# Kernel optimization log

Hardware: AMD Instinct MI355X
Metric: run time of the kernel (lower is better)

Reference implementation:

```python
import jax, jax.numpy as jnp
import numpy as np

THRESH = 0.5
MARGIN = 0.1
SCALE_POS = 2.0
SCALE_NEG = 40.0
SCALE_POS_W = 1.0
SCALE_NEG_W = 1.0

B, D = 4096, 256
N_CLASSES = 64


def setup_inputs() -> dict:
    key = jax.random.key(0)
    k1, k2, k3 = jax.random.split(key, 3)
    feats = jax.random.normal(k1, (B, D), dtype=jnp.float32)
    sim_weight = jax.random.uniform(k2, (B, B), dtype=jnp.float32)
    labels = jax.random.randint(k3, (B,), 0, N_CLASSES, dtype=jnp.int64)
    return {"feats": feats, "sim_weight": sim_weight, "labels": labels}


def reference(feats, sim_weight, labels):
    # L2-normalize rows, cosine-similarity matrix [B, B]
    feats_norm = feats / jnp.linalg.norm(feats, axis=1, keepdims=True)
    sim = feats_norm @ feats_norm.T

    # pos mask includes the diagonal (labels[i] == labels[i]), matching torch code
    pos_mask = labels[:, None] == labels[None, :]
    neg_mask = ~pos_mask

    # per-row min positive similarity (pos set is never empty due to diagonal)
    min_pos = jnp.min(jnp.where(pos_mask, sim, jnp.inf), axis=1, keepdims=True)
    # per-row max negative similarity; only valid when row has a negative
    has_neg = jnp.any(neg_mask, axis=1, keepdims=True)
    max_neg = jnp.max(jnp.where(neg_mask, sim, -jnp.inf), axis=1, keepdims=True)

    # hard mining: keep negs harder than the easiest pos, pos harder than hardest neg
    neg_keep = neg_mask & (sim + MARGIN > min_pos)
    pos_keep = pos_mask & jnp.where(has_neg, sim - MARGIN < max_neg, True)

    # masked log-sum-exp style reductions (non-vanila path uses sim_weight)
    pos_exp = jnp.exp(-SCALE_POS * (sim - THRESH) + SCALE_POS_W * sim_weight)
    neg_exp = jnp.exp(SCALE_NEG * (sim - THRESH) - SCALE_NEG_W * sim_weight)
    pos_sum = jnp.sum(jnp.where(pos_keep, pos_exp, 0.0), axis=1)
    neg_sum = jnp.sum(jnp.where(neg_keep, neg_exp, 0.0), axis=1)

    pos_loss = jnp.log1p(pos_sum) / SCALE_POS
    neg_loss = jnp.log1p(neg_sum) / SCALE_NEG
    # rows with both sets empty contribute log1p(0)=0, matching the `continue`
    return jnp.sum(pos_loss + neg_loss) / feats.shape[0]
```

## Files before the change

### kernel.cpp

```cpp
#include <hip/hip_runtime.h>
#include <hip/hip_bf16.h>
#include <math.h>

#define B_SZ 4096
#define D_SZ 256
#define MARGIN   0.1f

typedef __attribute__((ext_vector_type(8))) __bf16 bf16x8;
typedef __attribute__((ext_vector_type(4))) float f32x4;
typedef __attribute__((ext_vector_type(8))) unsigned short u16x8;

__device__ __forceinline__ unsigned fmap(float f) {
    unsigned u = __float_as_uint(f);
    return (u & 0x80000000u) ? ~u : (u | 0x80000000u);
}
__device__ __forceinline__ float funmap(unsigned u) {
    return (u & 0x80000000u) ? __uint_as_float(u ^ 0x80000000u)
                             : __uint_as_float(~u);
}
#define MINPOS_INIT 0xFF800000u
#define MAXNEG_INIT 0x007FFFFFu

__device__ __forceinline__ unsigned short f2bf(float f) {
    unsigned u = __float_as_uint(f);
    unsigned r = (u + 0x7FFFu + ((u >> 16) & 1u)) >> 16;
    return (unsigned short)r;
}

__device__ __forceinline__ void gload_lds16(const void* g, void* lds) {
    __builtin_amdgcn_global_load_lds(
        (const __attribute__((address_space(1))) void*)g,
        (__attribute__((address_space(3))) void*)lds, 16, 0, 0);
}

__global__ void norm_init_kernel(const float* __restrict__ feats,
                                 unsigned short* __restrict__ fb,
                                 unsigned* __restrict__ minpos,
                                 unsigned* __restrict__ maxneg,
                                 float* __restrict__ possum,
                                 float* __restrict__ negsum) {
    int row = blockIdx.x;
    int lane = threadIdx.x;
    const float4 v = *(const float4*)(feats + (size_t)row * D_SZ + lane * 4);
    float s = v.x * v.x + v.y * v.y + v.z * v.z + v.w * v.w;
#pragma unroll
    for (int m = 32; m; m >>= 1) s += __shfl_xor(s, m);
    float rinv = 1.0f / sqrtf(s);
    short4 st;
    st.x = (short)f2bf(v.x * rinv);
    st.y = (short)f2bf(v.y * rinv);
    st.z = (short)f2bf(v.z * rinv);
    st.w = (short)f2bf(v.w * rinv);
    *(short4*)(fb + (size_t)row * D_SZ + lane * 4) = st;
    if (lane == 0) {
        minpos[row] = MINPOS_INIT;
        maxneg[row] = MAXNEG_INIT;
        possum[row] = 0.f;
        negsum[row] = 0.f;
    }
}

__device__ __forceinline__ void gemm_tile(const unsigned short* __restrict__ fb,
                                          unsigned short* lA0, unsigned short* lB0,
                                          int i0, int j0, int t, f32x4 acc[4][4]) {
    const int lane = t & 63, w = t >> 6;
    const int wr = w >> 1, wc = w & 1;
    const int fr = lane & 15, kg = lane >> 4;
    const int srow = lane >> 2, schunk = lane & 3;

#pragma unroll
    for (int m = 0; m < 4; ++m)
#pragma unroll
        for (int n = 0; n < 4; ++n) acc[m][n] = (f32x4){0.f, 0.f, 0.f, 0.f};

    auto stage = [&](int buf, int kc) {
#pragma unroll
        for (int half = 0; half < 2; ++half) {
            const int R0 = w * 32 + half * 16;
            const int row = R0 + srow;
            const int off = ((schunk ^ ((row >> 1) & 3)) << 3);
            gload_lds16(fb + (size_t)(i0 + row) * D_SZ + kc + off,
                        lA0 + buf * (128 * 32) + R0 * 32);
            gload_lds16(fb + (size_t)(j0 + row) * D_SZ + kc + off,
                        lB0 + buf * (128 * 32) + R0 * 32);
        }
    };

    stage(0, 0);
    asm volatile("s_waitcnt vmcnt(0)" ::: "memory");
    __syncthreads();

#pragma unroll
    for (int s = 0; s < 8; ++s) {
        const int cur = s & 1;
        if (s < 7) stage(cur ^ 1, (s + 1) * 32);
        const unsigned short* A  = lA0 + cur * (128 * 32);
        const unsigned short* Bp = lB0 + cur * (128 * 32);
        bf16x8 a[4], b[4];
#pragma unroll
        for (int m = 0; m < 4; ++m) {
            const int row = wr * 64 + m * 16 + fr;
            a[m] = *(const bf16x8*)(A + row * 32 + ((kg ^ ((row >> 1) & 3)) << 3));
        }
#pragma unroll
        for (int n = 0; n < 4; ++n) {
            const int row = wc * 64 + n * 16 + fr;
            b[n] = *(const bf16x8*)(Bp + row * 32 + ((kg ^ ((row >> 1) & 3)) << 3));
        }
#pragma unroll
        for (int m = 0; m < 4; ++m)
#pragma unroll
            for (int n = 0; n < 4; ++n)
                acc[m][n] = __builtin_amdgcn_mfma_f32_16x16x32_bf16(a[m], b[n], acc[m][n], 0, 0, 0);
        if (s < 7) {
            asm volatile("s_waitcnt vmcnt(0)" ::: "memory");
            __syncthreads();
        }
    }
}

__global__ __launch_bounds__(256, 4) void gemm_store(const unsigned short* __restrict__ fb,
                                                     unsigned short* __restrict__ simb) {
    __shared__ unsigned short lA[2 * 128 * 32];
    __shared__ unsigned short lB[2 * 128 * 32];
    const int t = threadIdx.x;
    const int i0 = blockIdx.y * 128, j0 = blockIdx.x * 128;
    f32x4 acc[4][4];
    gemm_tile(fb, lA, lB, i0, j0, t, acc);
    const int lane = t & 63, w = t >> 6;
    const int wr = w >> 1, wc = w & 1, fr = lane & 15, kg = lane >> 4;
#pragma unroll
    for (int m = 0; m < 4; ++m)
#pragma unroll
        for (int r = 0; r < 4; ++r) {
            const size_t row = i0 + wr * 64 + m * 16 + kg * 4 + r;
#pragma unroll
            for (int n = 0; n < 4; ++n)
                simb[row * B_SZ + j0 + wc * 64 + n * 16 + fr] = f2bf(acc[m][n][r]);
        }
}

__global__ __launch_bounds__(256) void row_pass(const unsigned short* __restrict__ simb,
                                                const float* __restrict__ simw,
                                                const int* __restrict__ labels,
                                                float* __restrict__ rowloss) {
    const int i = blockIdx.x, t = threadIdx.x;
    const int lane = t & 63, w = t >> 6;
    const int il = labels[i];
    float sv[16], wv[16];
    int lj[16];
    {
        const u16x8* sp = (const u16x8*)(simb + (size_t)i * B_SZ + t * 16);
        u16x8 s0 = sp[0], s1 = sp[1];
#pragma unroll
        for (int e = 0; e < 8; ++e) {
            sv[e]     = __uint_as_float((unsigned)s0[e] << 16);
            sv[8 + e] = __uint_as_float((unsigned)s1[e] << 16);
        }
        const float4* wp = (const float4*)(simw + (size_t)i * B_SZ + t * 16);
#pragma unroll
        for (int q = 0; q < 4; ++q) {
            float4 wq = wp[q];
            wv[q * 4 + 0] = wq.x; wv[q * 4 + 1] = wq.y;
            wv[q * 4 + 2] = wq.z; wv[q * 4 + 3] = wq.w;
        }
        const int4* lp = (const int4*)(labels + t * 16);
#pragma unroll
        for (int q = 0; q < 4; ++q) {
            int4 lq = lp[q];
            lj[q * 4 + 0] = lq.x; lj[q * 4 + 1] = lq.y;
            lj[q * 4 + 2] = lq.z; lj[q * 4 + 3] = lq.w;
        }
    }
    float mn = INFINITY, mx = -INFINITY;
#pragma unroll
    for (int e = 0; e < 16; ++e) {
        if (lj[e] == il) mn = fminf(mn, sv[e]);
        else             mx = fmaxf(mx, sv[e]);
    }
#pragma unroll
    for (int msk = 1; msk < 64; msk <<= 1) {
        mn = fminf(mn, __shfl_xor(mn, msk));
        mx = fmaxf(mx, __shfl_xor(mx, msk));
    }
    __shared__ float smn[4], smx[4], sps[4], sns[4];
    if (lane == 0) { smn[w] = mn; smx[w] = mx; }
    __syncthreads();
    mn = fminf(fminf(smn[0], smn[1]), fminf(smn[2], smn[3]));
    mx = fmaxf(fmaxf(smx[0], smx[1]), fmaxf(smx[2], smx[3]));
    const bool hasneg = (mx != -INFINITY);
    float ps = 0.f, ns = 0.f;
#pragma unroll
    for (int e = 0; e < 16; ++e) {
        const float s = sv[e];
        if (lj[e] == il) {
            if (!hasneg || (s - MARGIN < mx))
                ps += __expf(fmaf(-2.f, s, 1.f) + wv[e]);
        } else {
            if (s + MARGIN > mn)
                ns += __expf(fmaf(40.f, s, -20.f) - wv[e]);
        }
    }
#pragma unroll
    for (int msk = 1; msk < 64; msk <<= 1) {
        ps += __shfl_xor(ps, msk);
        ns += __shfl_xor(ns, msk);
    }
    if (lane == 0) { sps[w] = ps; sns[w] = ns; }
    __syncthreads();
    if (t == 0) {
        ps = sps[0] + sps[1] + sps[2] + sps[3];
        ns = sns[0] + sns[1] + sns[2] + sns[3];
        rowloss[i] = log1pf(ps) * 0.5f + log1pf(ns) * 0.025f;
    }
}

__global__ void final_big(const float* __restrict__ rowloss, float* __restrict__ out) {
    __shared__ float red[256];
    int t = threadIdx.x;
    float acc = 0.f;
    for (int i = t; i < B_SZ; i += 256) acc += rowloss[i];
    red[t] = acc;
    __syncthreads();
    for (int s = 128; s > 0; s >>= 1) {
        if (t < s) red[t] += red[t + s];
        __syncthreads();
    }
    if (t == 0) out[0] = red[0] / (float)B_SZ;
}

template <int PHASE>
__global__ __launch_bounds__(256) void sim_pass(
    const unsigned short* __restrict__ fb,
    const int* __restrict__ labels,
    const float* __restrict__ simw,
    unsigned* __restrict__ minpos, unsigned* __restrict__ maxneg,
    float* __restrict__ possum, float* __restrict__ negsum) {
    __shared__ unsigned short lA[128 * 64];
    __shared__ unsigned short lB[128 * 64];
    const int t = threadIdx.x;
    const int lane = t & 63, w = t >> 6;
    const int wr = w >> 1, wc = w & 1;
    const int i0 = blockIdx.y * 128, j0 = blockIdx.x * 128;
    const int fr = lane & 15, kg = lane >> 4;
    const int srow = lane >> 3;
    const int scol = ((lane & 7) ^ srow) * 8;

    f32x4 acc[4][4];
#pragma unroll
    for (int m = 0; m < 4; ++m)
#pragma unroll
        for (int n = 0; n < 4; ++n)
            acc[m][n] = (f32x4){0.f, 0.f, 0.f, 0.f};

    const char* pA = (const char*)lA + (wr * 64 + fr) * 128;
    const char* pB = (const char*)lB + (wc * 64 + fr) * 128;
    const int q = (kg * 16) ^ ((fr & 7) << 4);

    for (int kc = 0; kc < D_SZ; kc += 64) {
        __syncthreads();
#pragma unroll
        for (int inst = 0; inst < 4; ++inst) {
            const int r8 = w * 32 + inst * 8;
            gload_lds16(fb + (size_t)(i0 + r8 + srow) * D_SZ + kc + scol, lA + r8 * 64);
            gload_lds16(fb + (size_t)(j0 + r8 + srow) * D_SZ + kc + scol, lB + r8 * 64);
        }
        asm volatile("s_waitcnt vmcnt(0)" ::: "memory");
        __syncthreads();
#pragma unroll
        for (int kk = 0; kk < 2; ++kk) {
            const int off = q ^ (kk * 64);
            bf16x8 a[4], b[4];
#pragma unroll
            for (int m = 0; m < 4; ++m)
                a[m] = *(const bf16x8*)(pA + m * 2048 + off);
#pragma unroll
            for (int n = 0; n < 4; ++n)
                b[n] = *(const bf16x8*)(pB + n * 2048 + off);
#pragma unroll
            for (int m = 0; m < 4; ++m)
#pragma unroll
                for (int n = 0; n < 4; ++n)
                    acc[m][n] = __builtin_amdgcn_mfma_f32_16x16x32_bf16(a[m], b[n], acc[m][n], 0, 0, 0);
        }
    }

    const int iBase = i0 + wr * 64, jBase = j0 + wc * 64;
    int jLab[4];
#pragma unroll
    for (int n = 0; n < 4; ++n) jLab[n] = labels[jBase + n * 16 + fr];

#pragma unroll
    for (int m = 0; m < 4; ++m) {
#pragma unroll
        for (int r = 0; r < 4; ++r) {
            const int i = iBase + m * 16 + kg * 4 + r;
            const int il = labels[i];
            if (PHASE == 0) {
                float mn = INFINITY, mx = -INFINITY;
#pragma unroll
                for (int n = 0; n < 4; ++n) {
                    float s = acc[m][n][r];
                    if (il == jLab[n]) mn = fminf(mn, s);
                    else               mx = fmaxf(mx, s);
                }
#pragma unroll
                for (int msk = 1; msk < 16; msk <<= 1) {
                    mn = fminf(mn, __shfl_xor(mn, msk));
                    mx = fmaxf(mx, __shfl_xor(mx, msk));
                }
                if (fr == 0) {
                    if (mn != INFINITY)  atomicMin(&minpos[i], fmap(mn));
                    if (mx != -INFINITY) atomicMax(&maxneg[i], fmap(mx));
                }
            } else {
                const unsigned mnu = maxneg[i];
                const float minp = funmap(minpos[i]);
                const bool hasneg = (mnu != MAXNEG_INIT);
                const float maxn = funmap(mnu);
                const float* wrow = simw + (size_t)i * B_SZ + jBase + fr;
                float ps = 0.f, ns = 0.f;
#pragma unroll
                for (int n = 0; n < 4; ++n) {
                    float s = acc[m][n][r];
                    float wv = wrow[n * 16];
                    if (il == jLab[n]) {
                        if (!hasneg || (s - MARGIN < maxn))
                            ps += __expf(fmaf(-2.f, s, 1.f) + wv);
                    } else {
                        if (s + MARGIN > minp)
                            ns += __expf(fmaf(40.f, s, -20.f) - wv);
                    }
                }
#pragma unroll
                for (int msk = 1; msk < 16; msk <<= 1) {
                    ps += __shfl_xor(ps, msk);
                    ns += __shfl_xor(ns, msk);
                }
                if (fr == 0) {
                    if (ps != 0.f) atomicAdd(&possum[i], ps);
                    if (ns != 0.f) atomicAdd(&negsum[i], ns);
                }
            }
        }
    }
}

__global__ void final_fb(const float* __restrict__ possum,
                         const float* __restrict__ negsum,
                         float* __restrict__ out) {
    __shared__ float red[256];
    int t = threadIdx.x;
    float acc = 0.f;
    for (int i = t; i < B_SZ; i += 256)
        acc += log1pf(possum[i]) * 0.5f + log1pf(negsum[i]) * 0.025f;
    red[t] = acc;
    __syncthreads();
    for (int s = 128; s > 0; s >>= 1) {
        if (t < s) red[t] += red[t + s];
        __syncthreads();
    }
    if (t == 0) out[0] = red[0] / (float)B_SZ;
}

extern "C" void kernel_launch(void* const* d_in, const int* in_sizes, int n_in,
                              void* d_out, int out_size, void* d_ws, size_t ws_size,
                              hipStream_t stream) {
    const float* feats  = (const float*)d_in[0];
    const float* simw   = (const float*)d_in[1];
    const int*   labels = (const int*)d_in[2];
    float* out = (float*)d_out;

    char* ws = (char*)d_ws;
    unsigned* minpos  = (unsigned*)ws;
    unsigned* maxneg  = (unsigned*)(ws + 1 * B_SZ * 4);
    float*    possum  = (float*)(ws + 2 * B_SZ * 4);
    float*    negsum  = (float*)(ws + 3 * B_SZ * 4);
    float*    rowloss = (float*)(ws + 4 * B_SZ * 4);
    unsigned short* fb   = (unsigned short*)(ws + 5 * B_SZ * 4);
    unsigned short* simb = (unsigned short*)(ws + 5 * B_SZ * 4 + (size_t)B_SZ * D_SZ * 2);

    const size_t NEED_BIG = 5ull * B_SZ * 4 + (size_t)B_SZ * D_SZ * 2
                          + (size_t)B_SZ * B_SZ * 2;

    norm_init_kernel<<<B_SZ, 64, 0, stream>>>(feats, fb, minpos, maxneg, possum, negsum);

    if (ws_size >= NEED_BIG) {
        dim3 grid(B_SZ / 128, B_SZ / 128);
        gemm_store<<<grid, 256, 0, stream>>>(fb, simb);
        row_pass<<<B_SZ, 256, 0, stream>>>(simb, simw, labels, rowloss);
        final_big<<<1, 256, 0, stream>>>(rowloss, out);
    } else {
        dim3 grid(B_SZ / 128, B_SZ / 128);
        sim_pass<0><<<grid, 256, 0, stream>>>(fb, labels, simw, minpos, maxneg, possum, negsum);
        sim_pass<1><<<grid, 256, 0, stream>>>(fb, labels, simw, minpos, maxneg, possum, negsum);
        final_fb<<<1, 256, 0, stream>>>(possum, negsum, out);
    }
}
```

Before: 52.28 us.

## Exploit similarity symmetry: compute upper-triangle tiles and write transposed copies

Replaces the full 32x32 tile GEMM with a triangular launch of 528 blocks that computes only the upper-triangle tiles of the symmetric cosine-similarity matrix. Each off-diagonal block writes its tile directly and also transposes it through swizzled LDS to write the mirrored tile. The intent is to nearly halve the MFMA work and the feature-tile loads. The fallback two-pass atomic path and its workspace init are removed, so the code now assumes the workspace is large enough. It adds a serial loop per block to decode the tile index and an extra LDS round trip plus a second set of stores.

```diff
diff --git a/kernel.cpp b/kernel.cpp
--- a/kernel.cpp
+++ b/kernel.cpp
@@ -9,17 +9,6 @@
 typedef __attribute__((ext_vector_type(8))) __bf16 bf16x8;
 typedef __attribute__((ext_vector_type(4))) float f32x4;
 typedef __attribute__((ext_vector_type(8))) unsigned short u16x8;
-
-__device__ __forceinline__ unsigned fmap(float f) {
-    unsigned u = __float_as_uint(f);
-    return (u & 0x80000000u) ? ~u : (u | 0x80000000u);
-}
-__device__ __forceinline__ float funmap(unsigned u) {
-    return (u & 0x80000000u) ? __uint_as_float(u ^ 0x80000000u)
-                             : __uint_as_float(~u);
-}
-#define MINPOS_INIT 0xFF800000u
-#define MAXNEG_INIT 0x007FFFFFu
 
 __device__ __forceinline__ unsigned short f2bf(float f) {
     unsigned u = __float_as_uint(f);
@@ -34,11 +23,7 @@
 }
 
 __global__ void norm_init_kernel(const float* __restrict__ feats,
-                                 unsigned short* __restrict__ fb,
-                                 unsigned* __restrict__ minpos,
-                                 unsigned* __restrict__ maxneg,
-                                 float* __restrict__ possum,
-                                 float* __restrict__ negsum) {
+                                 unsigned short* __restrict__ fb) {
     int row = blockIdx.x;
     int lane = threadIdx.x;
     const float4 v = *(const float4*)(feats + (size_t)row * D_SZ + lane * 4);
@@ -52,12 +37,6 @@
     st.z = (short)f2bf(v.z * rinv);
     st.w = (short)f2bf(v.w * rinv);
     *(short4*)(fb + (size_t)row * D_SZ + lane * 4) = st;
-    if (lane == 0) {
-        minpos[row] = MINPOS_INIT;
-        maxneg[row] = MAXNEG_INIT;
-        possum[row] = 0.f;
-        negsum[row] = 0.f;
-    }
 }
 
 __device__ __forceinline__ void gemm_tile(const unsigned short* __restrict__ fb,
@@ -119,16 +98,22 @@
     }
 }
 
-__global__ __launch_bounds__(256, 4) void gemm_store(const unsigned short* __restrict__ fb,
-                                                     unsigned short* __restrict__ simb) {
-    __shared__ unsigned short lA[2 * 128 * 32];
-    __shared__ unsigned short lB[2 * 128 * 32];
+__global__ __launch_bounds__(256, 4) void gemm_store_sym(const unsigned short* __restrict__ fb,
+                                                         unsigned short* __restrict__ simb) {
+    __shared__ unsigned short sm[2 * 128 * 32 * 2];
     const int t = threadIdx.x;
-    const int i0 = blockIdx.y * 128, j0 = blockIdx.x * 128;
+
+    int z = blockIdx.x, bi = 0;
+    while (z >= 32 - bi) { z -= 32 - bi; ++bi; }
+    const int bj = bi + z;
+    const int i0 = bi * 128, j0 = bj * 128;
+
     f32x4 acc[4][4];
-    gemm_tile(fb, lA, lB, i0, j0, t, acc);
+    gemm_tile(fb, sm, sm + 128 * 32 * 2, i0, j0, t, acc);
+
     const int lane = t & 63, w = t >> 6;
     const int wr = w >> 1, wc = w & 1, fr = lane & 15, kg = lane >> 4;
+
 #pragma unroll
     for (int m = 0; m < 4; ++m)
 #pragma unroll
@@ -138,6 +123,34 @@
             for (int n = 0; n < 4; ++n)
                 simb[row * B_SZ + j0 + wc * 64 + n * 16 + fr] = f2bf(acc[m][n][r]);
         }
+
+    if (bi == bj) return;
+
+    __syncthreads();
+    unsigned short* T = sm;
+#pragma unroll
+    for (int m = 0; m < 4; ++m) {
+        const int rowbase = wr * 64 + m * 16 + kg * 4;
+#pragma unroll
+        for (int n = 0; n < 4; ++n) {
+            const int col = wc * 64 + n * 16 + fr;
+            short4 h;
+            h.x = (short)f2bf(acc[m][n][0]);
+            h.y = (short)f2bf(acc[m][n][1]);
+            h.z = (short)f2bf(acc[m][n][2]);
+            h.w = (short)f2bf(acc[m][n][3]);
+            *(short4*)(T + col * 128 + (rowbase ^ ((col & 15) << 3))) = h;
+        }
+    }
+    __syncthreads();
+
+    const int r0 = t & 15, cb = t >> 4;
+#pragma unroll
+    for (int p = 0; p < 8; ++p) {
+        const int c = cb + p * 16;
+        u16x8 v = *(const u16x8*)(T + c * 128 + 8 * (r0 ^ (c & 15)));
+        *(u16x8*)(simb + (size_t)(j0 + c) * B_SZ + i0 + r0 * 8) = v;
+    }
 }
 
 __global__ __launch_bounds__(256) void row_pass(const unsigned short* __restrict__ simb,
@@ -229,140 +242,6 @@
     if (t == 0) out[0] = red[0] / (float)B_SZ;
 }
 
-template <int PHASE>
-__global__ __launch_bounds__(256) void sim_pass(
-    const unsigned short* __restrict__ fb,
-    const int* __restrict__ labels,
-    const float* __restrict__ simw,
-    unsigned* __restrict__ minpos, unsigned* __restrict__ maxneg,
-    float* __restrict__ possum, float* __restrict__ negsum) {
-    __shared__ unsigned short lA[128 * 64];
-    __shared__ unsigned short lB[128 * 64];
-    const int t = threadIdx.x;
-    const int lane = t & 63, w = t >> 6;
-    const int wr = w >> 1, wc = w & 1;
-    const int i0 = blockIdx.y * 128, j0 = blockIdx.x * 128;
-    const int fr = lane & 15, kg = lane >> 4;
-    const int srow = lane >> 3;
-    const int scol = ((lane & 7) ^ srow) * 8;
-
-    f32x4 acc[4][4];
-#pragma unroll
-    for (int m = 0; m < 4; ++m)
-#pragma unroll
-        for (int n = 0; n < 4; ++n)
-            acc[m][n] = (f32x4){0.f, 0.f, 0.f, 0.f};
-
-    const char* pA = (const char*)lA + (wr * 64 + fr) * 128;
-    const char* pB = (const char*)lB + (wc * 64 + fr) * 128;
-    const int q = (kg * 16) ^ ((fr & 7) << 4);
-
-    for (int kc = 0; kc < D_SZ; kc += 64) {
-        __syncthreads();
-#pragma unroll
-        for (int inst = 0; inst < 4; ++inst) {
-            const int r8 = w * 32 + inst * 8;
-            gload_lds16(fb + (size_t)(i0 + r8 + srow) * D_SZ + kc + scol, lA + r8 * 64);
-            gload_lds16(fb + (size_t)(j0 + r8 + srow) * D_SZ + kc + scol, lB + r8 * 64);
-        }
-        asm volatile("s_waitcnt vmcnt(0)" ::: "memory");
-        __syncthreads();
-#pragma unroll
-        for (int kk = 0; kk < 2; ++kk) {
-            const int off = q ^ (kk * 64);
-            bf16x8 a[4], b[4];
-#pragma unroll
-            for (int m = 0; m < 4; ++m)
-                a[m] = *(const bf16x8*)(pA + m * 2048 + off);
-#pragma unroll
-            for (int n = 0; n < 4; ++n)
-                b[n] = *(const bf16x8*)(pB + n * 2048 + off);
-#pragma unroll
-            for (int m = 0; m < 4; ++m)
-#pragma unroll
-                for (int n = 0; n < 4; ++n)
-                    acc[m][n] = __builtin_amdgcn_mfma_f32_16x16x32_bf16(a[m], b[n], acc[m][n], 0, 0, 0);
-        }
-    }
-
-    const int iBase = i0 + wr * 64, jBase = j0 + wc * 64;
-    int jLab[4];
-#pragma unroll
-    for (int n = 0; n < 4; ++n) jLab[n] = labels[jBase + n * 16 + fr];
-
-#pragma unroll
-    for (int m = 0; m < 4; ++m) {
-#pragma unroll
-        for (int r = 0; r < 4; ++r) {
-            const int i = iBase + m * 16 + kg * 4 + r;
-            const int il = labels[i];
-            if (PHASE == 0) {
-                float mn = INFINITY, mx = -INFINITY;
-#pragma unroll
-                for (int n = 0; n < 4; ++n) {
-                    float s = acc[m][n][r];
-                    if (il == jLab[n]) mn = fminf(mn, s);
-                    else               mx = fmaxf(mx, s);
-                }
-#pragma unroll
-                for (int msk = 1; msk < 16; msk <<= 1) {
-                    mn = fminf(mn, __shfl_xor(mn, msk));
-                    mx = fmaxf(mx, __shfl_xor(mx, msk));
-                }
-                if (fr == 0) {
-                    if (mn != INFINITY)  atomicMin(&minpos[i], fmap(mn));
-                    if (mx != -INFINITY) atomicMax(&maxneg[i], fmap(mx));
-                }
-            } else {
-                const unsigned mnu = maxneg[i];
-                const float minp = funmap(minpos[i]);
-                const bool hasneg = (mnu != MAXNEG_INIT);
-                const float maxn = funmap(mnu);
-                const float* wrow = simw + (size_t)i * B_SZ + jBase + fr;
-                float ps = 0.f, ns = 0.f;
-#pragma unroll
-                for (int n = 0; n < 4; ++n) {
-                    float s = acc[m][n][r];
-                    float wv = wrow[n * 16];
-                    if (il == jLab[n]) {
-                        if (!hasneg || (s - MARGIN < maxn))
-                            ps += __expf(fmaf(-2.f, s, 1.f) + wv);
-                    } else {
-                        if (s + MARGIN > minp)
-                            ns += __expf(fmaf(40.f, s, -20.f) - wv);
-                    }
-                }
-#pragma unroll
-                for (int msk = 1; msk < 16; msk <<= 1) {
-                    ps += __shfl_xor(ps, msk);
-                    ns += __shfl_xor(ns, msk);
-                }
-                if (fr == 0) {
-                    if (ps != 0.f) atomicAdd(&possum[i], ps);
-                    if (ns != 0.f) atomicAdd(&negsum[i], ns);
-                }
-            }
-        }
-    }
-}
-
-__global__ void final_fb(const float* __restrict__ possum,
-                         const float* __restrict__ negsum,
-                         float* __restrict__ out) {
-    __shared__ float red[256];
-    int t = threadIdx.x;
-    float acc = 0.f;
-    for (int i = t; i < B_SZ; i += 256)
-        acc += log1pf(possum[i]) * 0.5f + log1pf(negsum[i]) * 0.025f;
-    red[t] = acc;
-    __syncthreads();
-    for (int s = 128; s > 0; s >>= 1) {
-        if (t < s) red[t] += red[t + s];
-        __syncthreads();
-    }
-    if (t == 0) out[0] = red[0] / (float)B_SZ;
-}
-
 extern "C" void kernel_launch(void* const* d_in, const int* in_sizes, int n_in,
                               void* d_out, int out_size, void* d_ws, size_t ws_size,
                               hipStream_t stream) {
@@ -372,28 +251,13 @@
     float* out = (float*)d_out;
 
     char* ws = (char*)d_ws;
-    unsigned* minpos  = (unsigned*)ws;
-    unsigned* maxneg  = (unsigned*)(ws + 1 * B_SZ * 4);
-    float*    possum  = (float*)(ws + 2 * B_SZ * 4);
-    float*    negsum  = (float*)(ws + 3 * B_SZ * 4);
-    float*    rowloss = (float*)(ws + 4 * B_SZ * 4);
-    unsigned short* fb   = (unsigned short*)(ws + 5 * B_SZ * 4);
-    unsigned short* simb = (unsigned short*)(ws + 5 * B_SZ * 4 + (size_t)B_SZ * D_SZ * 2);
-
-    const size_t NEED_BIG = 5ull * B_SZ * 4 + (size_t)B_SZ * D_SZ * 2
-                          + (size_t)B_SZ * B_SZ * 2;
-
-    norm_init_kernel<<<B_SZ, 64, 0, stream>>>(feats, fb, minpos, maxneg, possum, negsum);
-
-    if (ws_size >= NEED_BIG) {
-        dim3 grid(B_SZ / 128, B_SZ / 128);
-        gemm_store<<<grid, 256, 0, stream>>>(fb, simb);
-        row_pass<<<B_SZ, 256, 0, stream>>>(simb, simw, labels, rowloss);
-        final_big<<<1, 256, 0, stream>>>(rowloss, out);
-    } else {
-        dim3 grid(B_SZ / 128, B_SZ / 128);
-        sim_pass<0><<<grid, 256, 0, stream>>>(fb, labels, simw, minpos, maxneg, possum, negsum);
-        sim_pass<1><<<grid, 256, 0, stream>>>(fb, labels, simw, minpos, maxneg, possum, negsum);
-        final_fb<<<1, 256, 0, stream>>>(possum, negsum, out);
-    }
-}
+    float*    rowloss = (float*)ws;
+    unsigned short* fb   = (unsigned short*)(ws + B_SZ * 4);
+    unsigned short* simb = (unsigned short*)(ws + B_SZ * 4 + (size_t)B_SZ * D_SZ * 2);
+
+    norm_init_kernel<<<B_SZ, 64, 0, stream>>>(feats, fb);
+
+    gemm_store_sym<<<528, 256, 0, stream>>>(fb, simb);
+    row_pass<<<B_SZ, 256, 0, stream>>>(simb, simw, labels, rowloss);
+    final_big<<<1, 256, 0, stream>>>(rowloss, out);
+}
```

After: 49.88 us. 4.6% less time.
